# Optimization experiments

Hardware: AMD Instinct MI355X
Metric: run time of the kernel (lower is better)

## Reference

```python
import jax, jax.numpy as jnp
import numpy as np

NEG_INF = -1e9  # matches the TF additive-mask constant


def setup_inputs() -> dict:
    key = jax.random.key(0)
    k1, k2, k3 = jax.random.split(key, 3)
    B, Tq, Tk, D = 8, 2048, 2048, 1024
    decoder_outputs = jax.random.normal(k1, (B, Tq, D), dtype=jnp.float32)
    encoder_outputs = jax.random.normal(k2, (B, Tk, D), dtype=jnp.float32)
    encoder_mask = jax.random.randint(k3, (B, Tk), 0, 2, dtype=jnp.int32)
    return {
        "decoder_outputs": decoder_outputs,
        "encoder_outputs": encoder_outputs,
        "encoder_mask": encoder_mask,
    }


def reference(decoder_outputs, encoder_outputs, encoder_mask):
    # score[b, q, k] = <dec[b, q], enc[b, k]>  (no 1/sqrt(d) scaling in original)
    score = jnp.einsum("bqd,bkd->bqk", decoder_outputs, encoder_outputs)
    m = encoder_mask.astype(score.dtype)[:, None, :]  # [B, 1, Tk]
    score = score + (1.0 - m) * NEG_INF
    attention_weights = jax.nn.softmax(score, axis=-1)
    context_vector = jnp.einsum("bqk,bkd->bqd", attention_weights, encoder_outputs)
    return (context_vector, attention_weights)
```

## Files before the change

kernel.cpp:

```cpp
#include <hip/hip_runtime.h>
#include <cstddef>
#include <cstdint>

typedef _Float16 f16x8 __attribute__((ext_vector_type(8)));
typedef _Float16 f16x4 __attribute__((ext_vector_type(4)));
typedef float f32x4 __attribute__((ext_vector_type(4)));

static constexpr int BATCH = 8;
static constexpr int TQ = 2048;
static constexpr int TK = 2048;
static constexpr int DIM = 1024;
static constexpr size_t CTX_ELEMS = (size_t)BATCH * TQ * DIM;
static constexpr size_t ATT_ELEMS = (size_t)BATCH * TQ * TK;

static constexpr size_t WS_DEC = 0;
static constexpr size_t WS_ENC = WS_DEC + CTX_ELEMS;
static constexpr size_t WS_ENCT = WS_ENC + CTX_ELEMS;
static constexpr size_t WS_W = WS_ENCT + CTX_ELEMS;
static constexpr size_t WS_NEEDED_BYTES = (WS_W + ATT_ELEMS) * 2;

__device__ __forceinline__ void async16(const void* g, const void* l) {
  __builtin_amdgcn_global_load_lds(
      (const __attribute__((address_space(1))) unsigned int*)g,
      (__attribute__((address_space(3))) unsigned int*)l, 16, 0, 0);
}

__device__ __forceinline__ f16x8 cvt8(float4 a, float4 b) {
  f16x8 h;
  h[0] = (_Float16)a.x; h[1] = (_Float16)a.y; h[2] = (_Float16)a.z; h[3] = (_Float16)a.w;
  h[4] = (_Float16)b.x; h[5] = (_Float16)b.y; h[6] = (_Float16)b.z; h[7] = (_Float16)b.w;
  return h;
}


__global__ __launch_bounds__(256) void convert_dec_kernel(
    const float* __restrict__ dec, _Float16* __restrict__ dec16) {
  size_t i = ((size_t)blockIdx.x * 256 + threadIdx.x) * 8;
  float4 a = *(const float4*)(dec + i);
  float4 b = *(const float4*)(dec + i + 4);
  *(f16x8*)(dec16 + i) = cvt8(a, b);
}

__global__ __launch_bounds__(256) void convert_enc_kernel(
    const float* __restrict__ enc, _Float16* __restrict__ enc16,
    _Float16* __restrict__ encT) {
  __shared__ _Float16 sT[64 * 72];
  const int k0 = blockIdx.x * 64, d0 = blockIdx.y * 64, b = blockIdx.z;
  const int t = threadIdx.x;
  const int krow = t >> 2;
  const int dcol = (t & 3) * 16;

  const float* src = enc + ((size_t)b * TK + k0 + krow) * DIM + d0 + dcol;
  float4 f0 = *(const float4*)(src);
  float4 f1 = *(const float4*)(src + 4);
  float4 f2 = *(const float4*)(src + 8);
  float4 f3 = *(const float4*)(src + 12);
  _Float16 h[16];
#pragma unroll
  for (int i = 0; i < 4; i++) {
    h[i]      = (_Float16)((&f0.x)[i]);
    h[i + 4]  = (_Float16)((&f1.x)[i]);
    h[i + 8]  = (_Float16)((&f2.x)[i]);
    h[i + 12] = (_Float16)((&f3.x)[i]);
  }
  _Float16* dsts = enc16 + ((size_t)b * TK + k0 + krow) * DIM + d0 + dcol;
  *(f16x8*)dsts = *(const f16x8*)&h[0];
  *(f16x8*)(dsts + 8) = *(const f16x8*)&h[8];
#pragma unroll
  for (int i = 0; i < 16; i++)
    sT[(dcol + i) * 72 + krow] = h[i];
  __syncthreads();

  const int drow = t >> 2;
  const int kg = (t & 3) * 16;
  f16x8 v0 = *(const f16x8*)&sT[drow * 72 + kg];
  f16x8 v1 = *(const f16x8*)&sT[drow * 72 + kg + 8];
  _Float16* dst = encT + ((size_t)b * DIM + d0 + drow) * TK + k0 + kg;
  *(f16x8*)dst = v0;
  *(f16x8*)(dst + 8) = v1;
}


template <int KD>
__device__ __forceinline__ void stage_half(const _Float16* __restrict__ Xb,
                                           _Float16* slot, int khalf,
                                           int w, int lane) {
  const int kgl = w & 3;
  const int rg0 = (w >> 2) * 2;
  const _Float16* g = Xb + (size_t)(rg0 * 64 + lane) * KD + khalf + kgl * 8;
  _Float16* l = slot + kgl * 2048 + rg0 * 512;
  async16(g, l);
  async16(g + (size_t)64 * KD, l + 512);
}

__device__ __forceinline__ void load4(f16x8 (&dst)[4], const _Float16* base) {
#pragma unroll
  for (int i = 0; i < 4; ++i) dst[i] = *(const f16x8*)(base + i * 128);
}

__device__ __forceinline__ void mfma16(f32x4 (&acc)[8][4], const f16x8 (&aF)[4],
                                       const f16x8 (&bF)[4], int mh) {
  __builtin_amdgcn_s_setprio(1);
#pragma unroll
  for (int i = 0; i < 4; ++i)
#pragma unroll
    for (int j = 0; j < 4; ++j)
      acc[mh * 4 + i][j] = __builtin_amdgcn_mfma_f32_16x16x32_f16(
          aF[i], bF[j], acc[mh * 4 + i][j], 0, 0, 0);
  __builtin_amdgcn_s_setprio(0);
}

template <int M, int N, int K>
__global__ __launch_bounds__(512, 2) void gemm8p(
    const _Float16* __restrict__ A, const _Float16* __restrict__ B,
    float* __restrict__ C) {
  __shared__ _Float16 lds[65536];
  constexpr int T = K / 64;

  const int b = blockIdx.x, nt = blockIdx.y, mt = blockIdx.z;
  const int tid = threadIdx.x;
  const int lane = tid & 63, w = tid >> 6;
  const int tm = lane & 15, quad = lane >> 4;
  const int wr = w >> 2, wc = w & 3;

  const _Float16* Ab = A + ((size_t)b * M + mt * 256) * K;
  const _Float16* Bb = B + ((size_t)b * N + nt * 256) * K;

  const int aBase = quad * 2048 + (wr * 128 + tm) * 8;
  const int bBase = quad * 2048 + (wc * 64 + tm) * 8;

  f32x4 acc[8][4] = {};

  stage_half<K>(Ab, lds, 0, w, lane);
  stage_half<K>(Bb, lds + 32768, 0, w, lane);
  stage_half<K>(Ab, lds + 16384, 32, w, lane);
  stage_half<K>(Bb, lds + 49152, 32, w, lane);
  stage_half<K>(Ab, lds + 8192, 64, w, lane);
  stage_half<K>(Bb, lds + 32768 + 8192, 64, w, lane);
  asm volatile("s_waitcnt vmcnt(8)" ::: "memory");
  __builtin_amdgcn_s_barrier();

  for (int t = 0; t < T; ++t) {
    const int p = t & 1, np = p ^ 1;
    _Float16* const aLo = lds + p * 8192;
    _Float16* const aHi = lds + 16384 + p * 8192;
    _Float16* const bLo = lds + 32768 + p * 8192;
    _Float16* const bHi = lds + 49152 + p * 8192;
    const bool s1 = (t + 1 < T), s2 = (t + 2 < T);
    f16x8 aF[4], bF[4];

    load4(aF, aLo + aBase);
    load4(bF, bLo + bBase);
    if (s1) stage_half<K>(Ab, lds + 16384 + np * 8192, (t + 1) * 64 + 32, w, lane);
    __builtin_amdgcn_s_barrier();
    mfma16(acc, aF, bF, 0);
    __builtin_amdgcn_s_barrier();

    load4(aF, aLo + aBase + 512);
    if (s1) {
      stage_half<K>(Bb, lds + 49152 + np * 8192, (t + 1) * 64 + 32, w, lane);
      asm volatile("s_waitcnt vmcnt(8)" ::: "memory");
    } else {
      asm volatile("s_waitcnt vmcnt(0)" ::: "memory");
    }
    __builtin_amdgcn_s_barrier();
    mfma16(acc, aF, bF, 1);
    __builtin_amdgcn_s_barrier();

    load4(aF, aHi + aBase);
    load4(bF, bHi + bBase);
    if (s2) stage_half<K>(Ab, lds + p * 8192, (t + 2) * 64, w, lane);
    __builtin_amdgcn_s_barrier();
    mfma16(acc, aF, bF, 0);
    __builtin_amdgcn_s_barrier();

    load4(aF, aHi + aBase + 512);
    if (s2) {
      stage_half<K>(Bb, lds + 32768 + p * 8192, (t + 2) * 64, w, lane);
      asm volatile("s_waitcnt vmcnt(8)" ::: "memory");
    } else if (t + 2 == T) {
      asm volatile("s_waitcnt vmcnt(4)" ::: "memory");
    }
    __builtin_amdgcn_s_barrier();
    mfma16(acc, aF, bF, 1);
    __builtin_amdgcn_s_barrier();
  }

#pragma unroll
  for (int i = 0; i < 8; ++i) {
#pragma unroll
    for (int rr = 0; rr < 4; ++rr) {
      size_t row = (size_t)b * M + mt * 256 + wr * 128 + i * 16 + quad * 4 + rr;
      float* Crow = C + row * (size_t)N + nt * 256 + wc * 64 + tm;
#pragma unroll
      for (int j = 0; j < 4; ++j) Crow[j * 16] = acc[i][j][rr];
    }
  }
}

__global__ __launch_bounds__(256) void softmax_kernel(
    float* __restrict__ S, const int* __restrict__ mask, _Float16* __restrict__ W16) {
  const int row = blockIdx.x;
  const int b = row >> 11;
  float* srow = S + (size_t)row * TK;
  const int* mrow = mask + (size_t)b * TK;
  const int t = threadIdx.x;

  float4 s0 = *(const float4*)(srow + t * 8);
  float4 s1 = *(const float4*)(srow + t * 8 + 4);
  int4 m0 = *(const int4*)(mrow + t * 8);
  int4 m1 = *(const int4*)(mrow + t * 8 + 4);

  float v[8] = {s0.x, s0.y, s0.z, s0.w, s1.x, s1.y, s1.z, s1.w};
  const int mm[8] = {m0.x, m0.y, m0.z, m0.w, m1.x, m1.y, m1.z, m1.w};
#pragma unroll
  for (int i = 0; i < 8; i++)
    if (!mm[i]) v[i] += -1e9f;

  float mx = v[0];
#pragma unroll
  for (int i = 1; i < 8; i++) mx = fmaxf(mx, v[i]);
#pragma unroll
  for (int off = 32; off > 0; off >>= 1) mx = fmaxf(mx, __shfl_down(mx, off));

  __shared__ float redm[4];
  __shared__ float reds[4];
  if ((t & 63) == 0) redm[t >> 6] = mx;
  __syncthreads();
  mx = fmaxf(fmaxf(redm[0], redm[1]), fmaxf(redm[2], redm[3]));

  float e[8];
  float lsum = 0.f;
#pragma unroll
  for (int i = 0; i < 8; i++) {
    e[i] = __expf(v[i] - mx);
    lsum += e[i];
  }
#pragma unroll
  for (int off = 32; off > 0; off >>= 1) lsum += __shfl_down(lsum, off);
  if ((t & 63) == 0) reds[t >> 6] = lsum;
  __syncthreads();
  const float inv = 1.0f / (reds[0] + reds[1] + reds[2] + reds[3]);

  float4 o0 = {e[0] * inv, e[1] * inv, e[2] * inv, e[3] * inv};
  float4 o1 = {e[4] * inv, e[5] * inv, e[6] * inv, e[7] * inv};
  *(float4*)(srow + t * 8) = o0;
  *(float4*)(srow + t * 8 + 4) = o1;
  if (W16) {
    f16x8 h;
    h[0] = (_Float16)o0.x; h[1] = (_Float16)o0.y; h[2] = (_Float16)o0.z; h[3] = (_Float16)o0.w;
    h[4] = (_Float16)o1.x; h[5] = (_Float16)o1.y; h[6] = (_Float16)o1.z; h[7] = (_Float16)o1.w;
    *(f16x8*)(W16 + (size_t)row * TK + t * 8) = h;
  }
}

static constexpr int BM = 128, BN = 128, BK = 32;
static constexpr int LDSS = 40;

__global__ __launch_bounds__(256) void score_kernel_fb(
    const float* __restrict__ dec, const float* __restrict__ enc,
    float* __restrict__ S) {
  __shared__ _Float16 sA[BM * LDSS];
  __shared__ _Float16 sB[BN * LDSS];
  const int nt = blockIdx.x, mt = blockIdx.y, b = blockIdx.z;
  const int t = threadIdx.x;
  const int lane = t & 63, wave = t >> 6;
  const int wm = wave >> 1, wn = wave & 1;
  const int tm = lane & 15, quad = lane >> 4;
  const float* Abase = dec + ((size_t)b * TQ + mt * BM) * DIM;
  const float* Bbase = enc + ((size_t)b * TK + nt * BN) * DIM;
  f32x4 acc[4][4] = {};
  const int r = t >> 2;
  const int c8 = (t & 3) * 8;
  for (int k0 = 0; k0 < DIM; k0 += BK) {
    float4 a0 = *(const float4*)(Abase + (size_t)r * DIM + k0 + c8);
    float4 a1 = *(const float4*)(Abase + (size_t)r * DIM + k0 + c8 + 4);
    float4 a2 = *(const float4*)(Abase + (size_t)(r + 64) * DIM + k0 + c8);
    float4 a3 = *(const float4*)(Abase + (size_t)(r + 64) * DIM + k0 + c8 + 4);
    float4 b0 = *(const float4*)(Bbase + (size_t)r * DIM + k0 + c8);
    float4 b1 = *(const float4*)(Bbase + (size_t)r * DIM + k0 + c8 + 4);
    float4 b2 = *(const float4*)(Bbase + (size_t)(r + 64) * DIM + k0 + c8);
    float4 b3 = *(const float4*)(Bbase + (size_t)(r + 64) * DIM + k0 + c8 + 4);
    __syncthreads();
    *(f16x8*)&sA[r * LDSS + c8] = cvt8(a0, a1);
    *(f16x8*)&sA[(r + 64) * LDSS + c8] = cvt8(a2, a3);
    *(f16x8*)&sB[r * LDSS + c8] = cvt8(b0, b1);
    *(f16x8*)&sB[(r + 64) * LDSS + c8] = cvt8(b2, b3);
    __syncthreads();
    f16x8 aF[4], bF[4];
#pragma unroll
    for (int i = 0; i < 4; i++)
      aF[i] = *(const f16x8*)&sA[(wm * 64 + i * 16 + tm) * LDSS + quad * 8];
#pragma unroll
    for (int j = 0; j < 4; j++)
      bF[j] = *(const f16x8*)&sB[(wn * 64 + j * 16 + tm) * LDSS + quad * 8];
#pragma unroll
    for (int i = 0; i < 4; i++)
#pragma unroll
      for (int j = 0; j < 4; j++)
        acc[i][j] = __builtin_amdgcn_mfma_f32_16x16x32_f16(aF[i], bF[j], acc[i][j], 0, 0, 0);
  }
#pragma unroll
  for (int i = 0; i < 4; i++) {
#pragma unroll
    for (int rr = 0; rr < 4; rr++) {
      size_t rowoff = ((size_t)b * TQ + mt * BM + wm * 64 + i * 16 + quad * 4 + rr) * (size_t)TK;
#pragma unroll
      for (int j = 0; j < 4; j++)
        S[rowoff + nt * BN + wn * 64 + j * 16 + tm] = acc[i][j][rr];
    }
  }
}

__global__ __launch_bounds__(256) void ctx_kernel_fb(
    const float* __restrict__ W, const float* __restrict__ enc,
    float* __restrict__ C) {
  __shared__ _Float16 sA[BM * LDSS];
  __shared__ _Float16 sB[BN * LDSS];
  const int nt = blockIdx.x;
  const int mt = blockIdx.y;
  const int b = blockIdx.z;
  const int t = threadIdx.x;
  const int lane = t & 63, wave = t >> 6;
  const int wm = wave >> 1, wn = wave & 1;
  const int tm = lane & 15, quad = lane >> 4;
  const float* Abase = W + ((size_t)b * TQ + mt * BM) * TK;
  const float* Ebase = enc + (size_t)b * TK * DIM + nt * BN;
  f32x4 acc[4][4] = {};
  const int r = t >> 2;
  const int c8 = (t & 3) * 8;
  const int kkB = (t & 7) * 4;
  const int nnB = (t >> 3) * 4;
  for (int k0 = 0; k0 < TK; k0 += BK) {
    float4 a0 = *(const float4*)(Abase + (size_t)r * TK + k0 + c8);
    float4 a1 = *(const float4*)(Abase + (size_t)r * TK + k0 + c8 + 4);
    float4 a2 = *(const float4*)(Abase + (size_t)(r + 64) * TK + k0 + c8);
    float4 a3 = *(const float4*)(Abase + (size_t)(r + 64) * TK + k0 + c8 + 4);
    float4 f[4];
#pragma unroll
    for (int i = 0; i < 4; i++)
      f[i] = *(const float4*)(Ebase + (size_t)(k0 + kkB + i) * DIM + nnB);
    __syncthreads();
    *(f16x8*)&sA[r * LDSS + c8] = cvt8(a0, a1);
    *(f16x8*)&sA[(r + 64) * LDSS + c8] = cvt8(a2, a3);
#pragma unroll
    for (int c = 0; c < 4; c++) {
      f16x4 h;
      h[0] = (_Float16)((&f[0].x)[c]);
      h[1] = (_Float16)((&f[1].x)[c]);
      h[2] = (_Float16)((&f[2].x)[c]);
      h[3] = (_Float16)((&f[3].x)[c]);
      *(f16x4*)&sB[(nnB + c) * LDSS + kkB] = h;
    }
    __syncthreads();
    f16x8 aF[4], bF[4];
#pragma unroll
    for (int i = 0; i < 4; i++)
      aF[i] = *(const f16x8*)&sA[(wm * 64 + i * 16 + tm) * LDSS + quad * 8];
#pragma unroll
    for (int j = 0; j < 4; j++)
      bF[j] = *(const f16x8*)&sB[(wn * 64 + j * 16 + tm) * LDSS + quad * 8];
#pragma unroll
    for (int i = 0; i < 4; i++)
#pragma unroll
      for (int j = 0; j < 4; j++)
        acc[i][j] = __builtin_amdgcn_mfma_f32_16x16x32_f16(aF[i], bF[j], acc[i][j], 0, 0, 0);
  }
#pragma unroll
  for (int i = 0; i < 4; i++) {
#pragma unroll
    for (int rr = 0; rr < 4; rr++) {
      size_t rowoff = ((size_t)b * TQ + mt * BM + wm * 64 + i * 16 + quad * 4 + rr) * (size_t)DIM;
#pragma unroll
      for (int j = 0; j < 4; j++)
        C[rowoff + nt * BN + wn * 64 + j * 16 + tm] = acc[i][j][rr];
    }
  }
}

extern "C" void kernel_launch(void* const* d_in, const int* in_sizes, int n_in,
                              void* d_out, int out_size, void* d_ws, size_t ws_size,
                              hipStream_t stream) {
  const float* dec = (const float*)d_in[0];
  const float* enc = (const float*)d_in[1];
  const int* mask = (const int*)d_in[2];

  float* ctx = (float*)d_out;
  float* attn = (float*)d_out + CTX_ELEMS;

  dim3 block(256);

  if (ws_size >= WS_NEEDED_BYTES) {
    _Float16* dec16 = (_Float16*)d_ws + WS_DEC;
    _Float16* enc16 = (_Float16*)d_ws + WS_ENC;
    _Float16* encT = (_Float16*)d_ws + WS_ENCT;
    _Float16* W16 = (_Float16*)d_ws + WS_W;

    convert_dec_kernel<<<dim3(CTX_ELEMS / (256 * 8)), block, 0, stream>>>(dec, dec16);
    convert_enc_kernel<<<dim3(TK / 64, DIM / 64, BATCH), block, 0, stream>>>(enc, enc16, encT);
    gemm8p<TQ, TK, DIM><<<dim3(BATCH, TK / 256, TQ / 256), dim3(512), 0, stream>>>(dec16, enc16, attn);
    softmax_kernel<<<dim3(BATCH * TQ), block, 0, stream>>>(attn, mask, W16);
    gemm8p<TQ, DIM, TK><<<dim3(BATCH, DIM / 256, TQ / 256), dim3(512), 0, stream>>>(W16, encT, ctx);
  } else {
    score_kernel_fb<<<dim3(TK / BN, TQ / BM, BATCH), block, 0, stream>>>(dec, enc, attn);
    softmax_kernel<<<dim3(BATCH * TQ), block, 0, stream>>>(attn, mask, nullptr);
    ctx_kernel_fb<<<dim3(DIM / BN, TQ / BM, BATCH), block, 0, stream>>>(attn, enc, ctx);
  }
}
```

Measured before the change: 514.0 us.

## Fuse decoder/encoder fp16 conversion and XOR-swizzle GEMM LDS tile layout

Merges the decoder conversion into the encoder convert/transpose kernel so one launch converts both inputs. Each block converts a 4096-element slice of the decoder. The GEMM's LDS staging also changes from a k-chunk-major layout to a row-major layout with 32 halves per row and an XOR swizzle on the 8-element chunk index. This targets LDS bank conflicts on the fragment reads. The risk is that the new swizzled indexing and async global-to-LDS addressing must match exactly.

```diff
diff --git a/kernel.cpp b/kernel.cpp
--- a/kernel.cpp
+++ b/kernel.cpp
@@ -33,17 +33,10 @@
 }
 
 
-__global__ __launch_bounds__(256) void convert_dec_kernel(
-    const float* __restrict__ dec, _Float16* __restrict__ dec16) {
-  size_t i = ((size_t)blockIdx.x * 256 + threadIdx.x) * 8;
-  float4 a = *(const float4*)(dec + i);
-  float4 b = *(const float4*)(dec + i + 4);
-  *(f16x8*)(dec16 + i) = cvt8(a, b);
-}
-
-__global__ __launch_bounds__(256) void convert_enc_kernel(
-    const float* __restrict__ enc, _Float16* __restrict__ enc16,
-    _Float16* __restrict__ encT) {
+__global__ __launch_bounds__(256) void convert_kernel(
+    const float* __restrict__ enc, const float* __restrict__ dec,
+    _Float16* __restrict__ enc16, _Float16* __restrict__ encT,
+    _Float16* __restrict__ dec16) {
   __shared__ _Float16 sT[64 * 72];
   const int k0 = blockIdx.x * 64, d0 = blockIdx.y * 64, b = blockIdx.z;
   const int t = threadIdx.x;
@@ -69,6 +62,18 @@
 #pragma unroll
   for (int i = 0; i < 16; i++)
     sT[(dcol + i) * 72 + krow] = h[i];
+
+  {
+    const int bid = ((blockIdx.z * gridDim.y) + blockIdx.y) * gridDim.x + blockIdx.x;
+    size_t base = (size_t)bid * 4096 + (size_t)t * 16;
+    float4 a0 = *(const float4*)(dec + base);
+    float4 a1 = *(const float4*)(dec + base + 4);
+    float4 a2 = *(const float4*)(dec + base + 8);
+    float4 a3 = *(const float4*)(dec + base + 12);
+    *(f16x8*)(dec16 + base) = cvt8(a0, a1);
+    *(f16x8*)(dec16 + base + 8) = cvt8(a2, a3);
+  }
+
   __syncthreads();
 
   const int drow = t >> 2;
@@ -82,20 +87,20 @@
 
 
 template <int KD>
-__device__ __forceinline__ void stage_half(const _Float16* __restrict__ Xb,
-                                           _Float16* slot, int khalf,
-                                           int w, int lane) {
-  const int kgl = w & 3;
-  const int rg0 = (w >> 2) * 2;
-  const _Float16* g = Xb + (size_t)(rg0 * 64 + lane) * KD + khalf + kgl * 8;
-  _Float16* l = slot + kgl * 2048 + rg0 * 512;
-  async16(g, l);
-  async16(g + (size_t)64 * KD, l + 512);
-}
-
-__device__ __forceinline__ void load4(f16x8 (&dst)[4], const _Float16* base) {
-#pragma unroll
-  for (int i = 0; i < 4; ++i) dst[i] = *(const f16x8*)(base + i * 128);
+__device__ __forceinline__ void stage_sub(const _Float16* __restrict__ Xb,
+                                          _Float16* slot, int khalf,
+                                          int w, int srow, int schunk) {
+#pragma unroll
+  for (int j = 0; j < 2; ++j) {
+    const int row0 = 16 * (j * 8 + w);
+    async16(Xb + (size_t)(row0 + srow) * KD + khalf + schunk * 8,
+            slot + row0 * 32);
+  }
+}
+
+__device__ __forceinline__ void load4s(f16x8 (&dst)[4], const _Float16* base) {
+#pragma unroll
+  for (int i = 0; i < 4; ++i) dst[i] = *(const f16x8*)(base + i * 512);
 }
 
 __device__ __forceinline__ void mfma16(f32x4 (&acc)[8][4], const f16x8 (&aF)[4],
@@ -126,17 +131,21 @@
   const _Float16* Ab = A + ((size_t)b * M + mt * 256) * K;
   const _Float16* Bb = B + ((size_t)b * N + nt * 256) * K;
 
-  const int aBase = quad * 2048 + (wr * 128 + tm) * 8;
-  const int bBase = quad * 2048 + (wc * 64 + tm) * 8;
+  const int srow = lane >> 2;
+  const int schunk = (lane & 3) ^ (srow & 3);
+
+  const int xorc = (quad ^ (tm & 3)) * 8;
+  const int aBase = (wr * 128 + tm) * 32 + xorc;
+  const int bBase = (wc * 64 + tm) * 32 + xorc;
 
   f32x4 acc[8][4] = {};
 
-  stage_half<K>(Ab, lds, 0, w, lane);
-  stage_half<K>(Bb, lds + 32768, 0, w, lane);
-  stage_half<K>(Ab, lds + 16384, 32, w, lane);
-  stage_half<K>(Bb, lds + 49152, 32, w, lane);
-  stage_half<K>(Ab, lds + 8192, 64, w, lane);
-  stage_half<K>(Bb, lds + 32768 + 8192, 64, w, lane);
+  stage_sub<K>(Ab, lds, 0, w, srow, schunk);
+  stage_sub<K>(Bb, lds + 32768, 0, w, srow, schunk);
+  stage_sub<K>(Ab, lds + 16384, 32, w, srow, schunk);
+  stage_sub<K>(Bb, lds + 49152, 32, w, srow, schunk);
+  stage_sub<K>(Ab, lds + 8192, 64, w, srow, schunk);
+  stage_sub<K>(Bb, lds + 32768 + 8192, 64, w, srow, schunk);
   asm volatile("s_waitcnt vmcnt(8)" ::: "memory");
   __builtin_amdgcn_s_barrier();
 
@@ -149,16 +158,16 @@
     const bool s1 = (t + 1 < T), s2 = (t + 2 < T);
     f16x8 aF[4], bF[4];
 
-    load4(aF, aLo + aBase);
-    load4(bF, bLo + bBase);
-    if (s1) stage_half<K>(Ab, lds + 16384 + np * 8192, (t + 1) * 64 + 32, w, lane);
+    load4s(aF, aLo + aBase);
+    load4s(bF, bLo + bBase);
+    if (s1) stage_sub<K>(Ab, lds + 16384 + np * 8192, (t + 1) * 64 + 32, w, srow, schunk);
     __builtin_amdgcn_s_barrier();
     mfma16(acc, aF, bF, 0);
     __builtin_amdgcn_s_barrier();
 
-    load4(aF, aLo + aBase + 512);
+    load4s(aF, aLo + aBase + 2048);
     if (s1) {
-      stage_half<K>(Bb, lds + 49152 + np * 8192, (t + 1) * 64 + 32, w, lane);
+      stage_sub<K>(Bb, lds + 49152 + np * 8192, (t + 1) * 64 + 32, w, srow, schunk);
       asm volatile("s_waitcnt vmcnt(8)" ::: "memory");
     } else {
       asm volatile("s_waitcnt vmcnt(0)" ::: "memory");
@@ -167,16 +176,16 @@
     mfma16(acc, aF, bF, 1);
     __builtin_amdgcn_s_barrier();
 
-    load4(aF, aHi + aBase);
-    load4(bF, bHi + bBase);
-    if (s2) stage_half<K>(Ab, lds + p * 8192, (t + 2) * 64, w, lane);
+    load4s(aF, aHi + aBase);
+    load4s(bF, bHi + bBase);
+    if (s2) stage_sub<K>(Ab, lds + p * 8192, (t + 2) * 64, w, srow, schunk);
     __builtin_amdgcn_s_barrier();
     mfma16(acc, aF, bF, 0);
     __builtin_amdgcn_s_barrier();
 
-    load4(aF, aHi + aBase + 512);
+    load4s(aF, aHi + aBase + 2048);
     if (s2) {
-      stage_half<K>(Bb, lds + 32768 + p * 8192, (t + 2) * 64, w, lane);
+      stage_sub<K>(Bb, lds + 32768 + p * 8192, (t + 2) * 64, w, srow, schunk);
       asm volatile("s_waitcnt vmcnt(8)" ::: "memory");
     } else if (t + 2 == T) {
       asm volatile("s_waitcnt vmcnt(4)" ::: "memory");
@@ -396,8 +405,8 @@
     _Float16* encT = (_Float16*)d_ws + WS_ENCT;
     _Float16* W16 = (_Float16*)d_ws + WS_W;
 
-    convert_dec_kernel<<<dim3(CTX_ELEMS / (256 * 8)), block, 0, stream>>>(dec, dec16);
-    convert_enc_kernel<<<dim3(TK / 64, DIM / 64, BATCH), block, 0, stream>>>(enc, enc16, encT);
+    convert_kernel<<<dim3(TK / 64, DIM / 64, BATCH), block, 0, stream>>>(
+        enc, dec, enc16, encT, dec16);
     gemm8p<TQ, TK, DIM><<<dim3(BATCH, TK / 256, TQ / 256), dim3(512), 0, stream>>>(dec16, enc16, attn);
     softmax_kernel<<<dim3(BATCH * TQ), block, 0, stream>>>(attn, mask, W16);
     gemm8p<TQ, DIM, TK><<<dim3(BATCH, DIM / 256, TQ / 256), dim3(512), 0, stream>>>(W16, encT, ctx);
```

Result: faster. 486.0 us (-5.5%).
